# Kernel optimization log

Measured on AMD Instinct MI355X. Metric: run time of the kernel, lower is better.

Reference implementation:

```python
import jax, jax.numpy as jnp
import numpy as np

EPS = 1e-5
K = 16  # neighbors

def bn(x, g, b):
    # BatchNorm in training mode: stats over all axes except the last (channel)
    ax = tuple(range(x.ndim - 1))
    m = x.mean(ax, keepdims=True)
    v = x.var(ax, keepdims=True)
    return g * (x - m) * jax.lax.rsqrt(v + EPS) + b

def setup_inputs() -> dict:
    key = jax.random.key(0)
    ks = jax.random.split(key, 12)
    B, N, M, C, D = 2, 16384, 4096, 32, 64
    H = D // 2
    p = lambda k, s: jax.random.normal(k, s, dtype=jnp.float32) * 0.1
    inp = {}
    inp["xyz"] = jax.random.normal(ks[0], (B, N, 3), dtype=jnp.float32)
    inp["feats"] = jax.random.normal(ks[1], (B, C, N), dtype=jnp.float32)
    inp["sample_idx"] = jax.random.randint(ks[2], (B, M), 0, N, dtype=jnp.int32)
    # RelativePosEncoder mlp: Conv2d(10, H, 1) + BN
    inp["W_pos"] = p(ks[3], (10, H)); inp["b_pos"] = jnp.zeros(H); inp["g_pos"] = jnp.ones(H); inp["be_pos"] = jnp.zeros(H)
    # feature_mlp: Conv2d(C, H, 1) + BN
    inp["W_feat"] = p(ks[4], (C, H)); inp["b_feat"] = jnp.zeros(H); inp["g_feat"] = jnp.ones(H); inp["be_feat"] = jnp.zeros(H)
    # attention score mlp: Conv2d(D, D, 1, bias=False)
    inp["W_score"] = p(ks[5], (D, D))
    # out_mlp: Conv1d(D, D, 1, bias=False) + BN
    inp["W_out"] = p(ks[6], (D, D)); inp["g_out"] = jnp.ones(D); inp["be_out"] = jnp.zeros(D)
    # LFA shortcut: Conv1d(C, D, 1, bias=False) + BN
    inp["W_sc1"] = p(ks[7], (C, D)); inp["g_sc1"] = jnp.ones(D); inp["be_sc1"] = jnp.zeros(D)
    # unit shortcut: Conv1d(C, D, 1, bias=False) + BN
    inp["W_sc2"] = p(ks[8], (C, D)); inp["g_sc2"] = jnp.ones(D); inp["be_sc2"] = jnp.zeros(D)
    return inp

def reference(xyz, feats, sample_idx,
              W_pos, b_pos, g_pos, be_pos,
              W_feat, b_feat, g_feat, be_feat,
              W_score,
              W_out, g_out, be_out,
              W_sc1, g_sc1, be_sc1,
              W_sc2, g_sc2, be_sc2):
    B, C, N = feats.shape
    featsT = jnp.transpose(feats, (0, 2, 1))                    # [B,N,C]
    xyz_ds = jnp.take_along_axis(xyz, sample_idx[:, :, None], axis=1)  # [B,M,3]
    # KNN: squared distances are monotone in cdist -> same topk indices
    d2 = jnp.sum((xyz_ds[:, :, None, :] - xyz[:, None, :, :]) ** 2, axis=-1)  # [B,M,N]
    _, knn_idx = jax.lax.top_k(-d2, K)                           # [B,M,K]
    gather = jax.vmap(lambda pts, idx: pts[idx])
    neigh_xyz = gather(xyz, knn_idx)                             # [B,M,K,3]
    neigh_feats = gather(featsT, knn_idx)                        # [B,M,K,C]
    center_feats = jnp.take_along_axis(featsT, sample_idx[:, :, None], axis=1)  # [B,M,C]
    # relative position encoding
    center = jnp.broadcast_to(xyz_ds[:, :, None, :], neigh_xyz.shape)
    rel = xyz_ds[:, :, None, :] - neigh_xyz                      # [B,M,K,3]
    dist = jnp.linalg.norm(rel, axis=-1, keepdims=True)          # [B,M,K,1]
    posf = jnp.concatenate([center, neigh_xyz, rel, dist], axis=-1)  # [B,M,K,10]
    pos_feats = jax.nn.relu(bn(posf @ W_pos + b_pos, g_pos, be_pos))       # [B,M,K,H]
    feat_feats = jax.nn.relu(bn(neigh_feats @ W_feat + b_feat, g_feat, be_feat))  # [B,M,K,H]
    combined = jnp.concatenate([feat_feats, pos_feats], axis=-1)  # [B,M,K,D]
    # attention pooling: softmax over the K (neighbor) axis
    scores = jax.nn.softmax(combined @ W_score, axis=2)
    pooled = jnp.sum(scores * combined, axis=2)                  # [B,M,D]
    out = jax.nn.relu(bn(pooled @ W_out, g_out, be_out))         # [B,M,D]
    sc1 = bn(jnp.mean(neigh_feats, axis=2) @ W_sc1, g_sc1, be_sc1)
    f_lfa = out + sc1
    f_sc = bn(center_feats @ W_sc2, g_sc2, be_sc2)
    y = jax.nn.relu(f_lfa + f_sc)                                # [B,M,D]
    return xyz_ds, jnp.transpose(y, (0, 2, 1)), sample_idx
```

## Files before the change

### kernel.cpp

```cpp
#include <hip/hip_runtime.h>
#include <math.h>

#define BB 2
#define NN 16384
#define MM 4096
#define C_IN 32
#define D_DIM 64
#define H_DIM 32
#define KNB 16
#define EPSV 1e-5f
#define FLT_BIG 3.0e38f
#define CAPK 128
#define NSPL 4
#define SPTS (NN / NSPL)

#define SPOS_SUM 0
#define SPOS_SQ 32
#define SFEAT_SUM 64
#define SFEAT_SQ 96
#define SSC1_SUM 128
#define SSC1_SQ 192
#define SSC2_SUM 256
#define SSC2_SQ 320
#define SOUT_SUM 384
#define SOUT_SQ 448
#define STATS_LEN 512
#define PA_W 384
#define PB_W 128
#define NBLK (BB * MM / 4)

typedef float f32x2 __attribute__((ext_vector_type(2)));

__device__ __forceinline__ f32x2 mk2_r21(float a, float b) {
    f32x2 r; r.x = a; r.y = b; return r;
}

__device__ __forceinline__ int clampi_r21(int v, int lo, int hi) {
    return v < lo ? lo : (v > hi ? hi : v);
}

__global__ __launch_bounds__(256) void prep_r21(const float* __restrict__ feats,
                                                const float* __restrict__ xyz,
                                                const int* __restrict__ sample_idx,
                                                float* __restrict__ featsT,
                                                float* __restrict__ xyz4,
                                                float* __restrict__ stats,
                                                float* __restrict__ out) {
    __shared__ float tile[C_IN][65];
    const int tid = threadIdx.x;
    const int b = blockIdx.x >> 8;
    const int n0 = (blockIdx.x & 255) * 64;
#pragma unroll
    for (int it = 0; it < 8; ++it) {
        int c = (tid >> 6) + 4 * it;
        int n = tid & 63;
        tile[c][n] = feats[((size_t)b * C_IN + c) * NN + n0 + n];
    }
    int e = blockIdx.x * 256 + tid;
    if (e < STATS_LEN) stats[e] = 0.f;
    if (e < BB * NN) {
        float x = xyz[e * 3 + 0], y = xyz[e * 3 + 1], z = xyz[e * 3 + 2];
        xyz4[e * 4 + 0] = x;
        xyz4[e * 4 + 1] = y;
        xyz4[e * 4 + 2] = z;
        xyz4[e * 4 + 3] = x * x + y * y + z * z;
    }
    if (e < BB * MM) {
        int bb2 = e >> 12;
        int sidx = clampi_r21(sample_idx[e], 0, NN - 1);
        const float* p = xyz + (size_t)(bb2 * NN + sidx) * 3;
        out[e * 3 + 0] = p[0];
        out[e * 3 + 1] = p[1];
        out[e * 3 + 2] = p[2];
        out[BB * MM * 3 + BB * D_DIM * MM + e] = (float)sample_idx[e];
    }
    __syncthreads();
#pragma unroll
    for (int it = 0; it < 8; ++it) {
        int c = tid & 31;
        int nn = (tid >> 5) + 8 * it;
        featsT[((size_t)b * NN + n0 + nn) * C_IN + c] = tile[c][nn];
    }
}

__device__ void knn_fullsplit_r21(const float* __restrict__ base4, int n0,
                                  float m2x, float m2y, float m2z, int lane,
                                  float* __restrict__ outd, int* __restrict__ outi) {
    float d2v[KNB]; int iv[KNB];
#pragma unroll
    for (int i = 0; i < KNB; i++) { d2v[i] = FLT_BIG; iv[i] = 0x7FFFFFFF; }
    float curmax = FLT_BIG; int amax = 0;
    for (int t = 0; t < SPTS / 64; ++t) {
        int n = n0 + lane + t * 64;
        const float4 p = *reinterpret_cast<const float4*>(base4 + (size_t)n * 4);
        float d2 = fmaf(p.x, m2x, p.w);
        d2 = fmaf(p.y, m2y, d2);
        d2 = fmaf(p.z, m2z, d2);
        if (d2 < curmax) {
#pragma unroll
            for (int i = 0; i < KNB; i++)
                if (i == amax) { d2v[i] = d2; iv[i] = n; }
            curmax = d2v[0]; amax = 0;
#pragma unroll
            for (int i = 1; i < KNB; i++)
                if (d2v[i] > curmax) { curmax = d2v[i]; amax = i; }
        }
    }
#pragma unroll
    for (int i = 0; i < KNB; i++) {
#pragma unroll
        for (int j = 0; j < KNB - 1; j++) {
            bool sw = (d2v[j] > d2v[j + 1]) ||
                      (d2v[j] == d2v[j + 1] && iv[j] > iv[j + 1]);
            if (sw) {
                float td = d2v[j]; d2v[j] = d2v[j + 1]; d2v[j + 1] = td;
                int   ti = iv[j];  iv[j]  = iv[j + 1];  iv[j + 1]  = ti;
            }
        }
    }
    float myd = FLT_BIG; int myidx = 0x7FFFFFFF;
#pragma unroll 1
    for (int r = 0; r < KNB; r++) {
        float cv = d2v[0]; int cid = iv[0]; int ml = lane;
#pragma unroll
        for (int off = 32; off > 0; off >>= 1) {
            float ov = __shfl_xor(cv, off);
            int   oid = __shfl_xor(cid, off);
            int   ol = __shfl_xor(ml, off);
            bool take = (ov < cv) || (ov == cv && oid < cid);
            cv = take ? ov : cv; cid = take ? oid : cid; ml = take ? ol : ml;
        }
        if (lane == r) { myd = cv; myidx = cid; }
        if (lane == ml) {
#pragma unroll
            for (int i = 0; i < KNB - 1; i++) { d2v[i] = d2v[i + 1]; iv[i] = iv[i + 1]; }
            d2v[KNB - 1] = FLT_BIG; iv[KNB - 1] = 0x7FFFFFFF;
        }
    }
    if (lane < KNB) { outd[lane] = myd; outi[lane] = myidx; }
}

__global__ __launch_bounds__(256) void knn_r21(const float* __restrict__ xyz4,
                                               const int* __restrict__ sample_idx,
                                               float* __restrict__ cand_d,
                                               int* __restrict__ cand_i) {
    __shared__ float bufd[16][CAPK];
    __shared__ int   bufi[16][CAPK];
    const int tid = threadIdx.x;
    const int w = tid >> 6, lane = tid & 63;
    const int split = blockIdx.x & (NSPL - 1);
    const int qgrp = blockIdx.x >> 2;
    const int qbase = qgrp * 16 + w * 4;
    const int b = qbase >> 12;
    const int n0 = split * SPTS;
    const float* base4 = xyz4 + (size_t)b * NN * 4;
    const float4* p4 = reinterpret_cast<const float4*>(base4) + n0 + lane;

    float m2x[4], m2y[4], m2z[4], md[4], v16[4];
#pragma unroll
    for (int j = 0; j < 4; j++) {
        int s = clampi_r21(sample_idx[qbase + j], 0, NN - 1);
        m2x[j] = -2.f * base4[(size_t)s * 4 + 0];
        m2y[j] = -2.f * base4[(size_t)s * 4 + 1];
        m2z[j] = -2.f * base4[(size_t)s * 4 + 2];
        md[j] = FLT_BIG;
    }
#pragma unroll 8
    for (int it = 0; it < SPTS / 64; ++it) {
        const float4 p = p4[(size_t)it * 64];
#pragma unroll
        for (int j = 0; j < 4; j++) {
            float t = fmaf(p.x, m2x[j], p.w);
            t = fmaf(p.y, m2y[j], t);
            t = fmaf(p.z, m2z[j], t);
            md[j] = fminf(md[j], t);
        }
    }
    {
        float sv[4];
#pragma unroll
        for (int j = 0; j < 4; j++) sv[j] = md[j];
#pragma unroll
        for (int k = 2; k <= 64; k <<= 1) {
#pragma unroll
            for (int j2 = k >> 1; j2 >= 1; j2 >>= 1) {
                const bool want_min = (((lane & j2) == 0) == ((lane & k) == 0));
#pragma unroll
                for (int j = 0; j < 4; j++) {
                    float ov = __shfl_xor(sv[j], j2);
                    float mn = fminf(sv[j], ov);
                    float mx = fmaxf(sv[j], ov);
                    sv[j] = want_min ? mn : mx;
                }
            }
        }
#pragma unroll
        for (int j = 0; j < 4; j++) v16[j] = __shfl(sv[j], KNB - 1);
    }
    int cnt[4] = {0, 0, 0, 0};
#pragma unroll 4
    for (int it = 0; it < SPTS / 64; ++it) {
        const float4 p = p4[(size_t)it * 64];
        const int n = n0 + lane + it * 64;
#pragma unroll
        for (int j = 0; j < 4; j++) {
            float t = fmaf(p.x, m2x[j], p.w);
            t = fmaf(p.y, m2y[j], t);
            t = fmaf(p.z, m2z[j], t);
            bool pred = (t <= v16[j]);
            unsigned long long bal = __ballot(pred);
            if (bal) {
                int pre = __builtin_amdgcn_mbcnt_hi((unsigned)(bal >> 32),
                          __builtin_amdgcn_mbcnt_lo((unsigned)bal, 0u));
                int pos = cnt[j] + pre;
                if (pred && pos < CAPK) {
                    bufd[w * 4 + j][pos] = t;
                    bufi[w * 4 + j][pos] = n;
                }
                cnt[j] += __popcll(bal);
            }
        }
    }
    {
        float dv[4]; int ivv[4];
#pragma unroll
        for (int j = 0; j < 4; j++) {
            const int qi = w * 4 + j;
            bool valid = (cnt[j] <= 64) && (lane < cnt[j]);
            dv[j]  = valid ? bufd[qi][lane] : FLT_BIG;
            ivv[j] = valid ? bufi[qi][lane] : 0x7FFFFFFF;
        }
#pragma unroll
        for (int k = 2; k <= 64; k <<= 1) {
#pragma unroll
            for (int j2 = k >> 1; j2 >= 1; j2 >>= 1) {
                const bool want_min = (((lane & j2) == 0) == ((lane & k) == 0));
#pragma unroll
                for (int j = 0; j < 4; j++) {
                    float od = __shfl_xor(dv[j], j2);
                    int   oi = __shfl_xor(ivv[j], j2);
                    bool mine_less = (dv[j] < od) || (dv[j] == od && ivv[j] < oi);
                    bool keep = (mine_less == want_min);
                    dv[j]  = keep ? dv[j]  : od;
                    ivv[j] = keep ? ivv[j] : oi;
                }
            }
        }
#pragma unroll 1
        for (int j = 0; j < 4; j++) {
            const int qi = w * 4 + j;
            const int q = qbase + j;
            float* outd = cand_d + ((size_t)q * NSPL + split) * KNB;
            int*   outi = cand_i + ((size_t)q * NSPL + split) * KNB;
            if (cnt[j] <= 64) {
                if (lane < KNB) { outd[lane] = dv[j]; outi[lane] = ivv[j]; }
            } else if (cnt[j] <= CAPK) {
#pragma unroll 1
                for (int half = 0; half < 2; ++half) {
                    int i = lane + 64 * half;
                    if (i < cnt[j]) {
                        float di = bufd[qi][i]; int xi = bufi[qi][i];
                        int rank = 0;
                        for (int t = 0; t < cnt[j]; ++t) {
                            float dt = bufd[qi][t]; int xt = bufi[qi][t];
                            rank += (dt < di || (dt == di && xt < xi)) ? 1 : 0;
                        }
                        if (rank < KNB) { outd[rank] = di; outi[rank] = xi; }
                    }
                }
            } else {
                knn_fullsplit_r21(base4, n0, m2x[j], m2y[j], m2z[j], lane, outd, outi);
            }
        }
    }
}

__device__ __forceinline__ void prebn_r21(const float (*posf)[12], const float (*nf)[C_IN],
                                          int k,
                                          const f32x2* __restrict__ wp2, float bp,
                                          const f32x2* __restrict__ wf2, float bf,
                                          float* a_out, float* f_out) {
    const f32x2* pp = reinterpret_cast<const f32x2*>(&posf[k][0]);
    f32x2 a2 = pp[0] * wp2[0];
    a2 = pp[1] * wp2[1] + a2;
    a2 = pp[2] * wp2[2] + a2;
    a2 = pp[3] * wp2[3] + a2;
    a2 = pp[4] * wp2[4] + a2;
    const f32x2* nn2 = reinterpret_cast<const f32x2*>(&nf[k][0]);
    f32x2 f2 = nn2[0] * wf2[0];
#pragma unroll
    for (int t = 1; t < 16; ++t) f2 = nn2[t] * wf2[t] + f2;
    *a_out = bp + a2.x + a2.y;
    *f_out = bf + f2.x + f2.y;
}

__global__ __launch_bounds__(256) void stageA_r21(const float* __restrict__ xyz4,
                                                  const int* __restrict__ sample_idx,
                                                  const float* __restrict__ featsT,
                                                  const float* __restrict__ cand_d,
                                                  const int* __restrict__ cand_i,
                                                  const float* __restrict__ W_pos, const float* __restrict__ b_pos,
                                                  const float* __restrict__ W_feat, const float* __restrict__ b_feat,
                                                  const float* __restrict__ W_sc1, const float* __restrict__ W_sc2,
                                                  float* __restrict__ combpre,
                                                  float* __restrict__ sc1_pre, float* __restrict__ sc2_pre,
                                                  float* __restrict__ partialsA) {
    __shared__ __align__(16) float posf[4][KNB][12];
    __shared__ __align__(16) float nf[4][KNB][C_IN];
    __shared__ float meanf[4][C_IN];
    __shared__ float centerf[4][C_IN];
    __shared__ float posS[4][H_DIM], posQ[4][H_DIM], featS[4][H_DIM], featQ[4][H_DIM];
    __shared__ float s1S[4][D_DIM], s1Q[4][D_DIM], s2S[4][D_DIM], s2Q[4][D_DIM];
    const int tid = threadIdx.x;
    const int w = tid >> 6, lane = tid & 63;
    const int q = blockIdx.x * 4 + w;
    const int b = q >> 12;
    const int sidx = clampi_r21(sample_idx[q], 0, NN - 1);
    const float* base4 = xyz4 + (size_t)b * NN * 4;

    float dmv; int imv;
    {
        const int run = lane >> 4, pos = lane & 15;
        const int ridx = (run & 1) ? (15 - pos) : pos;
        dmv = cand_d[(size_t)q * 64 + run * 16 + ridx];
        imv = cand_i[(size_t)q * 64 + run * 16 + ridx];
    }
    float qx = base4[(size_t)sidx * 4 + 0];
    float qy = base4[(size_t)sidx * 4 + 1];
    float qz = base4[(size_t)sidx * 4 + 2];
    if (lane < C_IN) centerf[w][lane] = featsT[((size_t)b * NN + sidx) * C_IN + lane];
#pragma unroll
    for (int k = 32; k <= 64; k <<= 1) {
#pragma unroll
        for (int j2 = k >> 1; j2 >= 1; j2 >>= 1) {
            const bool want_min = (((lane & j2) == 0) == ((lane & k) == 0));
            float od = __shfl_xor(dmv, j2);
            int   oi = __shfl_xor(imv, j2);
            bool mine_less = (dmv < od) || (dmv == od && imv < oi);
            bool keep = (mine_less == want_min);
            dmv = keep ? dmv : od;
            imv = keep ? imv : oi;
        }
    }

    if (lane < KNB) {
        int idx = clampi_r21(imv, 0, NN - 1);
        float nx = base4[(size_t)idx * 4 + 0];
        float ny = base4[(size_t)idx * 4 + 1];
        float nz = base4[(size_t)idx * 4 + 2];
        float rx = qx - nx, ry = qy - ny, rz = qz - nz;
        float dist = sqrtf(rx * rx + ry * ry + rz * rz);
        posf[w][lane][0] = qx; posf[w][lane][1] = qy; posf[w][lane][2] = qz;
        posf[w][lane][3] = nx; posf[w][lane][4] = ny; posf[w][lane][5] = nz;
        posf[w][lane][6] = rx; posf[w][lane][7] = ry; posf[w][lane][8] = rz;
        posf[w][lane][9] = dist; posf[w][lane][10] = 0.f; posf[w][lane][11] = 0.f;
    }
    const float* fT = featsT + (size_t)b * NN * C_IN;
#pragma unroll
    for (int ii = 0; ii < 2; ++ii) {
        int e4 = lane + 64 * ii;
        int k = e4 >> 3, c4 = e4 & 7;
        int idx = clampi_r21(__shfl(imv, k), 0, NN - 1);
        const float4 v = *reinterpret_cast<const float4*>(fT + (size_t)idx * C_IN + c4 * 4);
        *reinterpret_cast<float4*>(&nf[w][k][c4 * 4]) = v;
    }

    const int h = lane & 31;
    f32x2 wp2[5], wf2[16];
#pragma unroll
    for (int t = 0; t < 5; ++t)
        wp2[t] = mk2_r21(W_pos[(2 * t) * H_DIM + h], W_pos[(2 * t + 1) * H_DIM + h]);
#pragma unroll
    for (int t = 0; t < 16; ++t)
        wf2[t] = mk2_r21(W_feat[(2 * t) * H_DIM + h], W_feat[(2 * t + 1) * H_DIM + h]);
    const float bp = b_pos[h], bf = b_feat[h];

    float sP = 0.f, qP = 0.f, sF = 0.f, qF = 0.f;
    float* cp = combpre + (size_t)q * (KNB * D_DIM);
#pragma unroll
    for (int i2 = 0; i2 < 8; i2++) {
        int k = ((lane + 64 * i2) >> 5);
        float a, f;
        prebn_r21(posf[w], nf[w], k, wp2, bp, wf2, bf, &a, &f);
        sP += a; qP += a * a;
        sF += f; qF += f * f;
        cp[k * D_DIM + h] = f;
        cp[k * D_DIM + H_DIM + h] = a;
    }
    sP += __shfl_xor(sP, 32); qP += __shfl_xor(qP, 32);
    sF += __shfl_xor(sF, 32); qF += __shfl_xor(qF, 32);
    if (lane < H_DIM) {
        posS[w][h] = sP; posQ[w][h] = qP; featS[w][h] = sF; featQ[w][h] = qF;
    }
    if (lane < C_IN) {
        float s = 0.f;
#pragma unroll
        for (int k = 0; k < KNB; k++) s += nf[w][k][lane];
        meanf[w][lane] = s * (1.f / (float)KNB);
    }
    {
        float a = 0.f, c2 = 0.f;
#pragma unroll
        for (int j = 0; j < C_IN; j++) {
            a  += meanf[w][j]   * W_sc1[j * D_DIM + lane];
            c2 += centerf[w][j] * W_sc2[j * D_DIM + lane];
        }
        sc1_pre[(size_t)q * D_DIM + lane] = a;
        sc2_pre[(size_t)q * D_DIM + lane] = c2;
        s1S[w][lane] = a;  s1Q[w][lane] = a * a;
        s2S[w][lane] = c2; s2Q[w][lane] = c2 * c2;
    }
    __syncthreads();
    float* row = partialsA + (size_t)blockIdx.x * PA_W;
    if (tid < H_DIM) {
        row[SPOS_SUM + tid]  = posS[0][tid] + posS[1][tid] + posS[2][tid] + posS[3][tid];
        row[SPOS_SQ + tid]   = posQ[0][tid] + posQ[1][tid] + posQ[2][tid] + posQ[3][tid];
        row[SFEAT_SUM + tid] = featS[0][tid] + featS[1][tid] + featS[2][tid] + featS[3][tid];
        row[SFEAT_SQ + tid]  = featQ[0][tid] + featQ[1][tid] + featQ[2][tid] + featQ[3][tid];
    } else if (tid >= 64 && tid < 128) {
        int dd = tid - 64;
        row[SSC1_SUM + dd] = s1S[0][dd] + s1S[1][dd] + s1S[2][dd] + s1S[3][dd];
        row[SSC1_SQ + dd]  = s1Q[0][dd] + s1Q[1][dd] + s1Q[2][dd] + s1Q[3][dd];
    } else if (tid >= 128 && tid < 192) {
        int dd = tid - 128;
        row[SSC2_SUM + dd] = s2S[0][dd] + s2S[1][dd] + s2S[2][dd] + s2S[3][dd];
        row[SSC2_SQ + dd]  = s2Q[0][dd] + s2Q[1][dd] + s2Q[2][dd] + s2Q[3][dd];
    }
}

#define NRSPLIT 64
__global__ __launch_bounds__(256) void reduce_r21(const float* __restrict__ partials,
                                                  int rows, int width,
                                                  float* __restrict__ stats_out) {
    const int wchunks = (width + 255) / 256;
    const int wi = blockIdx.x % wchunks;
    const int pi = blockIdx.x / wchunks;
    const int c = wi * 256 + threadIdx.x;
    if (c >= width) return;
    const int per = rows / NRSPLIT;
    const int p0 = pi * per;
    float s = 0.f;
    for (int p = p0; p < p0 + per; ++p) s += partials[(size_t)p * width + c];
    atomicAdd(&stats_out[c], s);
}

__global__ __launch_bounds__(256) void stageB_r21(const float* __restrict__ combpre,
                                                  const float* __restrict__ g_pos, const float* __restrict__ be_pos,
                                                  const float* __restrict__ g_feat, const float* __restrict__ be_feat,
                                                  const float* __restrict__ W_score, const float* __restrict__ W_out,
                                                  const float* __restrict__ stats,
                                                  float* __restrict__ out_pre,
                                                  float* __restrict__ partialsB) {
    __shared__ __align__(16) float comb[4][KNB][D_DIM];
    __shared__ float scl[D_DIM], shf[D_DIM];
    __shared__ float pooled[4][D_DIM];
    __shared__ float oS[4][D_DIM], oQ[4][D_DIM];
    const int tid = threadIdx.x;
    const int w = tid >> 6, lane = tid & 63;
    const int q = blockIdx.x * 4 + w;

    if (tid < D_DIM) {
        const float inv1 = 1.f / (float)(BB * MM * KNB);
        float mean, var, g, bb;
        if (tid < H_DIM) {
            mean = stats[SFEAT_SUM + tid] * inv1;
            var  = fmaxf(stats[SFEAT_SQ + tid] * inv1 - mean * mean, 0.f);
            g = g_feat[tid]; bb = be_feat[tid];
        } else {
            int h = tid - H_DIM;
            mean = stats[SPOS_SUM + h] * inv1;
            var  = fmaxf(stats[SPOS_SQ + h] * inv1 - mean * mean, 0.f);
            g = g_pos[h]; bb = be_pos[h];
        }
        float s = g * rsqrtf(var + EPSV);
        scl[tid] = s;
        shf[tid] = bb - mean * s;
    }
    __syncthreads();

    const float4* src = reinterpret_cast<const float4*>(combpre + (size_t)blockIdx.x * 4 * KNB * D_DIM);
#pragma unroll
    for (int i = 0; i < 4; ++i) {
        int f = tid + 256 * i;
        int qloc = f >> 8;
        int k = (f >> 4) & 15;
        int j4 = f & 15;
        float4 v = src[f];
        int j = j4 * 4;
        v.x = fmaxf(v.x * scl[j + 0] + shf[j + 0], 0.f);
        v.y = fmaxf(v.y * scl[j + 1] + shf[j + 1], 0.f);
        v.z = fmaxf(v.z * scl[j + 2] + shf[j + 2], 0.f);
        v.w = fmaxf(v.w * scl[j + 3] + shf[j + 3], 0.f);
        *reinterpret_cast<float4*>(&comb[qloc][k][j]) = v;
    }
    __syncthreads();

    const int d = lane;
    f32x2 s2[KNB];
#pragma unroll
    for (int k = 0; k < KNB; k++) s2[k] = mk2_r21(0.f, 0.f);
#pragma unroll 4
    for (int j4 = 0; j4 < D_DIM / 4; ++j4) {
        f32x2 wA = mk2_r21(W_score[(j4 * 4 + 0) * D_DIM + d],
                           W_score[(j4 * 4 + 1) * D_DIM + d]);
        f32x2 wB = mk2_r21(W_score[(j4 * 4 + 2) * D_DIM + d],
                           W_score[(j4 * 4 + 3) * D_DIM + d]);
#pragma unroll
        for (int k = 0; k < KNB; k++) {
            const f32x2* cb = reinterpret_cast<const f32x2*>(&comb[w][k][j4 * 4]);
            s2[k] = cb[0] * wA + s2[k];
            s2[k] = cb[1] * wB + s2[k];
        }
    }
    float s[KNB];
#pragma unroll
    for (int k = 0; k < KNB; k++) s[k] = s2[k].x + s2[k].y;
    float mx = s[0];
#pragma unroll
    for (int k = 1; k < KNB; k++) mx = fmaxf(mx, s[k]);
    float sum = 0.f;
#pragma unroll
    for (int k = 0; k < KNB; k++) { s[k] = __expf(s[k] - mx); sum += s[k]; }
    float inv = 1.f / sum;
    float pv = 0.f;
#pragma unroll
    for (int k = 0; k < KNB; k++) pv += s[k] * inv * comb[w][k][d];
    pooled[w][d] = pv;
    __syncthreads();
    float o = 0.f;
#pragma unroll
    for (int dd = 0; dd < D_DIM; dd++) o += pooled[w][dd] * W_out[dd * D_DIM + d];
    out_pre[(size_t)q * D_DIM + d] = o;
    oS[w][d] = o; oQ[w][d] = o * o;
    __syncthreads();
    float* row = partialsB + (size_t)blockIdx.x * PB_W;
    if (tid < D_DIM) {
        row[tid] = oS[0][tid] + oS[1][tid] + oS[2][tid] + oS[3][tid];
    } else if (tid < 2 * D_DIM) {
        int dd = tid - D_DIM;
        row[D_DIM + dd] = oQ[0][dd] + oQ[1][dd] + oQ[2][dd] + oQ[3][dd];
    }
}

__global__ __launch_bounds__(256) void final_r21(const float* __restrict__ out_pre,
                                                 const float* __restrict__ sc1_pre,
                                                 const float* __restrict__ sc2_pre,
                                                 const float* __restrict__ stats,
                                                 const float* __restrict__ g_out, const float* __restrict__ be_out,
                                                 const float* __restrict__ g_sc1, const float* __restrict__ be_sc1,
                                                 const float* __restrict__ g_sc2, const float* __restrict__ be_sc2,
                                                 float* __restrict__ out) {
    __shared__ float yt[64][65];
    const int tid = threadIdx.x;
    const int blk = blockIdx.x;
    const int b = blk >> 6;
    const int m0 = (blk & 63) * 64;
    const int d = tid & 63;

    const float invn = 1.f / (float)(BB * MM);
    float mo = stats[SOUT_SUM + d] * invn;
    float vo = fmaxf(stats[SOUT_SQ + d] * invn - mo * mo, 0.f);
    float so = g_out[d] * rsqrtf(vo + EPSV);
    float oo = be_out[d] - mo * so;
    float m1 = stats[SSC1_SUM + d] * invn;
    float v1 = fmaxf(stats[SSC1_SQ + d] * invn - m1 * m1, 0.f);
    float s1 = g_sc1[d] * rsqrtf(v1 + EPSV);
    float o1 = be_sc1[d] - m1 * s1;
    float m2 = stats[SSC2_SUM + d] * invn;
    float v2 = fmaxf(stats[SSC2_SQ + d] * invn - m2 * m2, 0.f);
    float s2 = g_sc2[d] * rsqrtf(v2 + EPSV);
    float o2 = be_sc2[d] - m2 * s2;

#pragma unroll
    for (int p = 0; p < 16; p++) {
        int ml = (tid >> 6) + 4 * p;
        size_t q = (size_t)b * MM + m0 + ml;
        float x_out = fmaxf(out_pre[q * D_DIM + d] * so + oo, 0.f);
        float x1 = sc1_pre[q * D_DIM + d] * s1 + o1;
        float x2 = sc2_pre[q * D_DIM + d] * s2 + o2;
        yt[ml][d] = fmaxf(x_out + x1 + x2, 0.f);
    }
    __syncthreads();
#pragma unroll
    for (int p = 0; p < 16; p++) {
        int dr = (tid >> 6) + 4 * p;
        int mc = tid & 63;
        out[BB * MM * 3 + (size_t)b * (D_DIM * MM) + (size_t)dr * MM + m0 + mc] = yt[mc][dr];
    }
}

extern "C" void kernel_launch(void* const* d_in, const int* in_sizes, int n_in,
                              void* d_out, int out_size, void* d_ws, size_t ws_size,
                              hipStream_t stream) {
    const float* xyz        = (const float*)d_in[0];
    const float* feats      = (const float*)d_in[1];
    const int*   sample_idx = (const int*)d_in[2];
    const float* W_pos  = (const float*)d_in[3];
    const float* b_pos  = (const float*)d_in[4];
    const float* g_pos  = (const float*)d_in[5];
    const float* be_pos = (const float*)d_in[6];
    const float* W_feat  = (const float*)d_in[7];
    const float* b_feat  = (const float*)d_in[8];
    const float* g_feat  = (const float*)d_in[9];
    const float* be_feat = (const float*)d_in[10];
    const float* W_score = (const float*)d_in[11];
    const float* W_out  = (const float*)d_in[12];
    const float* g_out  = (const float*)d_in[13];
    const float* be_out = (const float*)d_in[14];
    const float* W_sc1  = (const float*)d_in[15];
    const float* g_sc1  = (const float*)d_in[16];
    const float* be_sc1 = (const float*)d_in[17];
    const float* W_sc2  = (const float*)d_in[18];
    const float* g_sc2  = (const float*)d_in[19];
    const float* be_sc2 = (const float*)d_in[20];

    float* out = (float*)d_out;
    float* ws = (float*)d_ws;

    float* featsT    = ws;
    float* xyz4      = featsT + 1048576;
    float* sc1_pre   = xyz4 + 131072;
    float* sc2_pre   = sc1_pre + 524288;
    float* out_pre   = sc2_pre + 524288;
    float* stats     = out_pre + 524288;
    float* partialsA = stats + STATS_LEN;
    float* partialsB = partialsA + NBLK * PA_W;
    float* cand_d    = partialsB + NBLK * PB_W;
    int*   cand_i    = (int*)(cand_d + (size_t)BB * MM * NSPL * KNB);
    float* combpre   = (float*)(cand_i + (size_t)BB * MM * NSPL * KNB);

    prep_r21<<<BB * (NN / 64), 256, 0, stream>>>(feats, xyz, sample_idx,
                                                 featsT, xyz4, stats, out);

    knn_r21<<<(BB * MM / 16) * NSPL, 256, 0, stream>>>(xyz4, sample_idx, cand_d, cand_i);

    stageA_r21<<<NBLK, 256, 0, stream>>>(xyz4, sample_idx, featsT, cand_d, cand_i,
                                         W_pos, b_pos, W_feat, b_feat, W_sc1, W_sc2,
                                         combpre, sc1_pre, sc2_pre, partialsA);
    reduce_r21<<<2 * NRSPLIT, 256, 0, stream>>>(partialsA, NBLK, PA_W, stats);

    stageB_r21<<<NBLK, 256, 0, stream>>>(combpre,
                                         g_pos, be_pos, g_feat, be_feat,
                                         W_score, W_out, stats, out_pre, partialsB);
    reduce_r21<<<1 * NRSPLIT, 256, 0, stream>>>(partialsB, NBLK, PB_W, stats + SOUT_SUM);

    final_r21<<<BB * (MM / 64), 256, 0, stream>>>(out_pre, sc1_pre, sc2_pre, stats,
                                                  g_out, be_out, g_sc1, be_sc1, g_sc2, be_sc2, out);
}
```

Baseline: 235.7 us.

## Split KNN into bound and collect kernels; replace partial reductions with atomics

The KNN kernel is split in two. A separate kernel computes each query's per-split 16th-smallest bound and writes it to a buffer, and a second kernel reads that bound and collects candidates. Separately, the per-block BatchNorm statistics partials and the two reduce kernels are removed; stageA and stageB now atomically add block sums straight into the stats buffer. This drops two launches and the partials traffic, at the cost of an extra KNN launch and an extra small global buffer round trip. It also risks atomic contention on a few hundred addresses from 2048 blocks.

```diff
diff --git a/kernel.cpp b/kernel.cpp
--- a/kernel.cpp
+++ b/kernel.cpp
@@ -31,15 +31,15 @@
 
 typedef float f32x2 __attribute__((ext_vector_type(2)));
 
-__device__ __forceinline__ f32x2 mk2_r21(float a, float b) {
+__device__ __forceinline__ f32x2 mk2_r22(float a, float b) {
     f32x2 r; r.x = a; r.y = b; return r;
 }
 
-__device__ __forceinline__ int clampi_r21(int v, int lo, int hi) {
+__device__ __forceinline__ int clampi_r22(int v, int lo, int hi) {
     return v < lo ? lo : (v > hi ? hi : v);
 }
 
-__global__ __launch_bounds__(256) void prep_r21(const float* __restrict__ feats,
+__global__ __launch_bounds__(256) void prep_r22(const float* __restrict__ feats,
                                                 const float* __restrict__ xyz,
                                                 const int* __restrict__ sample_idx,
                                                 float* __restrict__ featsT,
@@ -67,7 +67,7 @@
     }
     if (e < BB * MM) {
         int bb2 = e >> 12;
-        int sidx = clampi_r21(sample_idx[e], 0, NN - 1);
+        int sidx = clampi_r22(sample_idx[e], 0, NN - 1);
         const float* p = xyz + (size_t)(bb2 * NN + sidx) * 3;
         out[e * 3 + 0] = p[0];
         out[e * 3 + 1] = p[1];
@@ -83,7 +83,67 @@
     }
 }
 
-__device__ void knn_fullsplit_r21(const float* __restrict__ base4, int n0,
+__global__ __launch_bounds__(256) void knn_bound_r22(const float* __restrict__ xyz4,
+                                                     const int* __restrict__ sample_idx,
+                                                     float* __restrict__ v16buf) {
+    const int tid = threadIdx.x;
+    const int w = tid >> 6, lane = tid & 63;
+    const int split = blockIdx.x & (NSPL - 1);
+    const int qgrp = blockIdx.x >> 2;
+    const int qbase = qgrp * 16 + w * 4;
+    const int b = qbase >> 12;
+    const int n0 = split * SPTS;
+    const float* base4 = xyz4 + (size_t)b * NN * 4;
+    const float4* p4 = reinterpret_cast<const float4*>(base4) + n0 + lane;
+
+    float m2x[4], m2y[4], m2z[4], md[4];
+#pragma unroll
+    for (int j = 0; j < 4; j++) {
+        int s = clampi_r22(sample_idx[qbase + j], 0, NN - 1);
+        m2x[j] = -2.f * base4[(size_t)s * 4 + 0];
+        m2y[j] = -2.f * base4[(size_t)s * 4 + 1];
+        m2z[j] = -2.f * base4[(size_t)s * 4 + 2];
+        md[j] = FLT_BIG;
+    }
+#pragma unroll 8
+    for (int it = 0; it < SPTS / 64; ++it) {
+        const float4 p = p4[(size_t)it * 64];
+#pragma unroll
+        for (int j = 0; j < 4; j++) {
+            float t = fmaf(p.x, m2x[j], p.w);
+            t = fmaf(p.y, m2y[j], t);
+            t = fmaf(p.z, m2z[j], t);
+            md[j] = fminf(md[j], t);
+        }
+    }
+    float sv[4];
+#pragma unroll
+    for (int j = 0; j < 4; j++) sv[j] = md[j];
+#pragma unroll
+    for (int k = 2; k <= 64; k <<= 1) {
+#pragma unroll
+        for (int j2 = k >> 1; j2 >= 1; j2 >>= 1) {
+            const bool want_min = (((lane & j2) == 0) == ((lane & k) == 0));
+#pragma unroll
+            for (int j = 0; j < 4; j++) {
+                float ov = __shfl_xor(sv[j], j2);
+                float mn = fminf(sv[j], ov);
+                float mx = fmaxf(sv[j], ov);
+                sv[j] = want_min ? mn : mx;
+            }
+        }
+    }
+    float v0 = __shfl(sv[0], KNB - 1);
+    float v1 = __shfl(sv[1], KNB - 1);
+    float v2 = __shfl(sv[2], KNB - 1);
+    float v3 = __shfl(sv[3], KNB - 1);
+    if (lane < 4) {
+        float v = (lane == 0) ? v0 : (lane == 1) ? v1 : (lane == 2) ? v2 : v3;
+        v16buf[(size_t)(qbase + lane) * NSPL + split] = v;
+    }
+}
+
+__device__ void knn_fullsplit_r22(const float* __restrict__ base4, int n0,
                                   float m2x, float m2y, float m2z, int lane,
                                   float* __restrict__ outd, int* __restrict__ outi) {
     float d2v[KNB]; int iv[KNB];
@@ -140,10 +200,11 @@
     if (lane < KNB) { outd[lane] = myd; outi[lane] = myidx; }
 }
 
-__global__ __launch_bounds__(256) void knn_r21(const float* __restrict__ xyz4,
-                                               const int* __restrict__ sample_idx,
-                                               float* __restrict__ cand_d,
-                                               int* __restrict__ cand_i) {
+__global__ __launch_bounds__(256) void knn_coll_r22(const float* __restrict__ xyz4,
+                                                    const int* __restrict__ sample_idx,
+                                                    const float* __restrict__ v16buf,
+                                                    float* __restrict__ cand_d,
+                                                    int* __restrict__ cand_i) {
     __shared__ float bufd[16][CAPK];
     __shared__ int   bufi[16][CAPK];
     const int tid = threadIdx.x;
@@ -156,46 +217,14 @@
     const float* base4 = xyz4 + (size_t)b * NN * 4;
     const float4* p4 = reinterpret_cast<const float4*>(base4) + n0 + lane;
 
-    float m2x[4], m2y[4], m2z[4], md[4], v16[4];
+    float m2x[4], m2y[4], m2z[4], v16[4];
 #pragma unroll
     for (int j = 0; j < 4; j++) {
-        int s = clampi_r21(sample_idx[qbase + j], 0, NN - 1);
+        int s = clampi_r22(sample_idx[qbase + j], 0, NN - 1);
         m2x[j] = -2.f * base4[(size_t)s * 4 + 0];
         m2y[j] = -2.f * base4[(size_t)s * 4 + 1];
         m2z[j] = -2.f * base4[(size_t)s * 4 + 2];
-        md[j] = FLT_BIG;
-    }
-#pragma unroll 8
-    for (int it = 0; it < SPTS / 64; ++it) {
-        const float4 p = p4[(size_t)it * 64];
-#pragma unroll
-        for (int j = 0; j < 4; j++) {
-            float t = fmaf(p.x, m2x[j], p.w);
-            t = fmaf(p.y, m2y[j], t);
-            t = fmaf(p.z, m2z[j], t);
-            md[j] = fminf(md[j], t);
-        }
-    }
-    {
-        float sv[4];
-#pragma unroll
-        for (int j = 0; j < 4; j++) sv[j] = md[j];
-#pragma unroll
-        for (int k = 2; k <= 64; k <<= 1) {
-#pragma unroll
-            for (int j2 = k >> 1; j2 >= 1; j2 >>= 1) {
-                const bool want_min = (((lane & j2) == 0) == ((lane & k) == 0));
-#pragma unroll
-                for (int j = 0; j < 4; j++) {
-                    float ov = __shfl_xor(sv[j], j2);
-                    float mn = fminf(sv[j], ov);
-                    float mx = fmaxf(sv[j], ov);
-                    sv[j] = want_min ? mn : mx;
-                }
-            }
-        }
-#pragma unroll
-        for (int j = 0; j < 4; j++) v16[j] = __shfl(sv[j], KNB - 1);
+        v16[j] = v16buf[(size_t)(qbase + j) * NSPL + split];
     }
     int cnt[4] = {0, 0, 0, 0};
 #pragma unroll 4
@@ -269,13 +298,13 @@
                     }
                 }
             } else {
-                knn_fullsplit_r21(base4, n0, m2x[j], m2y[j], m2z[j], lane, outd, outi);
+                knn_fullsplit_r22(base4, n0, m2x[j], m2y[j], m2z[j], lane, outd, outi);
             }
         }
     }
 }
 
-__device__ __forceinline__ void prebn_r21(const float (*posf)[12], const float (*nf)[C_IN],
+__device__ __forceinline__ void prebn_r22(const float (*posf)[12], const float (*nf)[C_IN],
                                           int k,
                                           const f32x2* __restrict__ wp2, float bp,
                                           const f32x2* __restrict__ wf2, float bf,
@@ -294,7 +323,7 @@
     *f_out = bf + f2.x + f2.y;
 }
 
-__global__ __launch_bounds__(256) void stageA_r21(const float* __restrict__ xyz4,
+__global__ __launch_bounds__(256) void stageA_r22(const float* __restrict__ xyz4,
                                                   const int* __restrict__ sample_idx,
                                                   const float* __restrict__ featsT,
                                                   const float* __restrict__ cand_d,
@@ -304,7 +333,7 @@
                                                   const float* __restrict__ W_sc1, const float* __restrict__ W_sc2,
                                                   float* __restrict__ combpre,
                                                   float* __restrict__ sc1_pre, float* __restrict__ sc2_pre,
-                                                  float* __restrict__ partialsA) {
+                                                  float* __restrict__ stats) {
     __shared__ __align__(16) float posf[4][KNB][12];
     __shared__ __align__(16) float nf[4][KNB][C_IN];
     __shared__ float meanf[4][C_IN];
@@ -315,7 +344,7 @@
     const int w = tid >> 6, lane = tid & 63;
     const int q = blockIdx.x * 4 + w;
     const int b = q >> 12;
-    const int sidx = clampi_r21(sample_idx[q], 0, NN - 1);
+    const int sidx = clampi_r22(sample_idx[q], 0, NN - 1);
     const float* base4 = xyz4 + (size_t)b * NN * 4;
 
     float dmv; int imv;
@@ -344,7 +373,7 @@
     }
 
     if (lane < KNB) {
-        int idx = clampi_r21(imv, 0, NN - 1);
+        int idx = clampi_r22(imv, 0, NN - 1);
         float nx = base4[(size_t)idx * 4 + 0];
         float ny = base4[(size_t)idx * 4 + 1];
         float nz = base4[(size_t)idx * 4 + 2];
@@ -360,7 +389,7 @@
     for (int ii = 0; ii < 2; ++ii) {
         int e4 = lane + 64 * ii;
         int k = e4 >> 3, c4 = e4 & 7;
-        int idx = clampi_r21(__shfl(imv, k), 0, NN - 1);
+        int idx = clampi_r22(__shfl(imv, k), 0, NN - 1);
         const float4 v = *reinterpret_cast<const float4*>(fT + (size_t)idx * C_IN + c4 * 4);
         *reinterpret_cast<float4*>(&nf[w][k][c4 * 4]) = v;
     }
@@ -369,10 +398,10 @@
     f32x2 wp2[5], wf2[16];
 #pragma unroll
     for (int t = 0; t < 5; ++t)
-        wp2[t] = mk2_r21(W_pos[(2 * t) * H_DIM + h], W_pos[(2 * t + 1) * H_DIM + h]);
+        wp2[t] = mk2_r22(W_pos[(2 * t) * H_DIM + h], W_pos[(2 * t + 1) * H_DIM + h]);
 #pragma unroll
     for (int t = 0; t < 16; ++t)
-        wf2[t] = mk2_r21(W_feat[(2 * t) * H_DIM + h], W_feat[(2 * t + 1) * H_DIM + h]);
+        wf2[t] = mk2_r22(W_feat[(2 * t) * H_DIM + h], W_feat[(2 * t + 1) * H_DIM + h]);
     const float bp = b_pos[h], bf = b_feat[h];
 
     float sP = 0.f, qP = 0.f, sF = 0.f, qF = 0.f;
@@ -381,7 +410,7 @@
     for (int i2 = 0; i2 < 8; i2++) {
         int k = ((lane + 64 * i2) >> 5);
         float a, f;
-        prebn_r21(posf[w], nf[w], k, wp2, bp, wf2, bf, &a, &f);
+        prebn_r22(posf[w], nf[w], k, wp2, bp, wf2, bf, &a, &f);
         sP += a; qP += a * a;
         sF += f; qF += f * f;
         cp[k * D_DIM + h] = f;
@@ -411,46 +440,28 @@
         s2S[w][lane] = c2; s2Q[w][lane] = c2 * c2;
     }
     __syncthreads();
-    float* row = partialsA + (size_t)blockIdx.x * PA_W;
     if (tid < H_DIM) {
-        row[SPOS_SUM + tid]  = posS[0][tid] + posS[1][tid] + posS[2][tid] + posS[3][tid];
-        row[SPOS_SQ + tid]   = posQ[0][tid] + posQ[1][tid] + posQ[2][tid] + posQ[3][tid];
-        row[SFEAT_SUM + tid] = featS[0][tid] + featS[1][tid] + featS[2][tid] + featS[3][tid];
-        row[SFEAT_SQ + tid]  = featQ[0][tid] + featQ[1][tid] + featQ[2][tid] + featQ[3][tid];
+        atomicAdd(&stats[SPOS_SUM + tid],  posS[0][tid] + posS[1][tid] + posS[2][tid] + posS[3][tid]);
+        atomicAdd(&stats[SPOS_SQ + tid],   posQ[0][tid] + posQ[1][tid] + posQ[2][tid] + posQ[3][tid]);
+        atomicAdd(&stats[SFEAT_SUM + tid], featS[0][tid] + featS[1][tid] + featS[2][tid] + featS[3][tid]);
+        atomicAdd(&stats[SFEAT_SQ + tid],  featQ[0][tid] + featQ[1][tid] + featQ[2][tid] + featQ[3][tid]);
     } else if (tid >= 64 && tid < 128) {
         int dd = tid - 64;
-        row[SSC1_SUM + dd] = s1S[0][dd] + s1S[1][dd] + s1S[2][dd] + s1S[3][dd];
-        row[SSC1_SQ + dd]  = s1Q[0][dd] + s1Q[1][dd] + s1Q[2][dd] + s1Q[3][dd];
+        atomicAdd(&stats[SSC1_SUM + dd], s1S[0][dd] + s1S[1][dd] + s1S[2][dd] + s1S[3][dd]);
+        atomicAdd(&stats[SSC1_SQ + dd],  s1Q[0][dd] + s1Q[1][dd] + s1Q[2][dd] + s1Q[3][dd]);
     } else if (tid >= 128 && tid < 192) {
         int dd = tid - 128;
-        row[SSC2_SUM + dd] = s2S[0][dd] + s2S[1][dd] + s2S[2][dd] + s2S[3][dd];
-        row[SSC2_SQ + dd]  = s2Q[0][dd] + s2Q[1][dd] + s2Q[2][dd] + s2Q[3][dd];
-    }
-}
-
-#define NRSPLIT 64
-__global__ __launch_bounds__(256) void reduce_r21(const float* __restrict__ partials,
-                                                  int rows, int width,
-                                                  float* __restrict__ stats_out) {
-    const int wchunks = (width + 255) / 256;
-    const int wi = blockIdx.x % wchunks;
-    const int pi = blockIdx.x / wchunks;
-    const int c = wi * 256 + threadIdx.x;
-    if (c >= width) return;
-    const int per = rows / NRSPLIT;
-    const int p0 = pi * per;
-    float s = 0.f;
-    for (int p = p0; p < p0 + per; ++p) s += partials[(size_t)p * width + c];
-    atomicAdd(&stats_out[c], s);
-}
-
-__global__ __launch_bounds__(256) void stageB_r21(const float* __restrict__ combpre,
+        atomicAdd(&stats[SSC2_SUM + dd], s2S[0][dd] + s2S[1][dd] + s2S[2][dd] + s2S[3][dd]);
+        atomicAdd(&stats[SSC2_SQ + dd],  s2Q[0][dd] + s2Q[1][dd] + s2Q[2][dd] + s2Q[3][dd]);
+    }
+}
+
+__global__ __launch_bounds__(256) void stageB_r22(const float* __restrict__ combpre,
                                                   const float* __restrict__ g_pos, const float* __restrict__ be_pos,
                                                   const float* __restrict__ g_feat, const float* __restrict__ be_feat,
                                                   const float* __restrict__ W_score, const float* __restrict__ W_out,
-                                                  const float* __restrict__ stats,
-                                                  float* __restrict__ out_pre,
-                                                  float* __restrict__ partialsB) {
+                                                  float* __restrict__ stats,
+                                                  float* __restrict__ out_pre) {
     __shared__ __align__(16) float comb[4][KNB][D_DIM];
     __shared__ float scl[D_DIM], shf[D_DIM];
     __shared__ float pooled[4][D_DIM];
@@ -498,12 +509,12 @@
     const int d = lane;
     f32x2 s2[KNB];
 #pragma unroll
-    for (int k = 0; k < KNB; k++) s2[k] = mk2_r21(0.f, 0.f);
+    for (int k = 0; k < KNB; k++) s2[k] = mk2_r22(0.f, 0.f);
 #pragma unroll 4
     for (int j4 = 0; j4 < D_DIM / 4; ++j4) {
-        f32x2 wA = mk2_r21(W_score[(j4 * 4 + 0) * D_DIM + d],
+        f32x2 wA = mk2_r22(W_score[(j4 * 4 + 0) * D_DIM + d],
                            W_score[(j4 * 4 + 1) * D_DIM + d]);
-        f32x2 wB = mk2_r21(W_score[(j4 * 4 + 2) * D_DIM + d],
+        f32x2 wB = mk2_r22(W_score[(j4 * 4 + 2) * D_DIM + d],
                            W_score[(j4 * 4 + 3) * D_DIM + d]);
 #pragma unroll
         for (int k = 0; k < KNB; k++) {
@@ -533,16 +544,15 @@
     out_pre[(size_t)q * D_DIM + d] = o;
     oS[w][d] = o; oQ[w][d] = o * o;
     __syncthreads();
-    float* row = partialsB + (size_t)blockIdx.x * PB_W;
     if (tid < D_DIM) {
-        row[tid] = oS[0][tid] + oS[1][tid] + oS[2][tid] + oS[3][tid];
+        atomicAdd(&stats[SOUT_SUM + tid], oS[0][tid] + oS[1][tid] + oS[2][tid] + oS[3][tid]);
     } else if (tid < 2 * D_DIM) {
         int dd = tid - D_DIM;
-        row[D_DIM + dd] = oQ[0][dd] + oQ[1][dd] + oQ[2][dd] + oQ[3][dd];
-    }
-}
-
-__global__ __launch_bounds__(256) void final_r21(const float* __restrict__ out_pre,
+        atomicAdd(&stats[SOUT_SQ + dd], oQ[0][dd] + oQ[1][dd] + oQ[2][dd] + oQ[3][dd]);
+    }
+}
+
+__global__ __launch_bounds__(256) void final_r22(const float* __restrict__ out_pre,
                                                  const float* __restrict__ sc1_pre,
                                                  const float* __restrict__ sc2_pre,
                                                  const float* __restrict__ stats,
@@ -623,27 +633,27 @@
     float* sc2_pre   = sc1_pre + 524288;
     float* out_pre   = sc2_pre + 524288;
     float* stats     = out_pre + 524288;
-    float* partialsA = stats + STATS_LEN;
-    float* partialsB = partialsA + NBLK * PA_W;
-    float* cand_d    = partialsB + NBLK * PB_W;
+    float* v16buf    = stats + STATS_LEN;
+    float* cand_d    = v16buf + 131072;
     int*   cand_i    = (int*)(cand_d + (size_t)BB * MM * NSPL * KNB);
     float* combpre   = (float*)(cand_i + (size_t)BB * MM * NSPL * KNB);
 
-    prep_r21<<<BB * (NN / 64), 256, 0, stream>>>(feats, xyz, sample_idx,
+    prep_r22<<<BB * (NN / 64), 256, 0, stream>>>(feats, xyz, sample_idx,
                                                  featsT, xyz4, stats, out);
 
-    knn_r21<<<(BB * MM / 16) * NSPL, 256, 0, stream>>>(xyz4, sample_idx, cand_d, cand_i);
-
-    stageA_r21<<<NBLK, 256, 0, stream>>>(xyz4, sample_idx, featsT, cand_d, cand_i,
+    knn_bound_r22<<<(BB * MM / 16) * NSPL, 256, 0, stream>>>(xyz4, sample_idx, v16buf);
+
+    knn_coll_r22<<<(BB * MM / 16) * NSPL, 256, 0, stream>>>(xyz4, sample_idx, v16buf,
+                                                            cand_d, cand_i);
+
+    stageA_r22<<<NBLK, 256, 0, stream>>>(xyz4, sample_idx, featsT, cand_d, cand_i,
                                          W_pos, b_pos, W_feat, b_feat, W_sc1, W_sc2,
-                                         combpre, sc1_pre, sc2_pre, partialsA);
-    reduce_r21<<<2 * NRSPLIT, 256, 0, stream>>>(partialsA, NBLK, PA_W, stats);
-
-    stageB_r21<<<NBLK, 256, 0, stream>>>(combpre,
+                                         combpre, sc1_pre, sc2_pre, stats);
+
+    stageB_r22<<<NBLK, 256, 0, stream>>>(combpre,
                                          g_pos, be_pos, g_feat, be_feat,
-                                         W_score, W_out, stats, out_pre, partialsB);
-    reduce_r21<<<1 * NRSPLIT, 256, 0, stream>>>(partialsB, NBLK, PB_W, stats + SOUT_SUM);
-
-    final_r21<<<BB * (MM / 64), 256, 0, stream>>>(out_pre, sc1_pre, sc2_pre, stats,
+                                         W_score, W_out, stats, out_pre);
+
+    final_r22<<<BB * (MM / 64), 256, 0, stream>>>(out_pre, sc1_pre, sc2_pre, stats,
                                                   g_out, be_out, g_sc1, be_sc1, g_sc2, be_sc2, out);
 }
```

New measurement: 295.4 us. +25.3%, slower.
